# Optimization experiments

Hardware: AMD Instinct MI355X
Metric: run time of the kernel (lower is better)

Reference implementation:

```python
import jax, jax.numpy as jnp
import numpy as np

D_MODEL = 768
NUM_HEADS = 12
HEAD_DIM = D_MODEL // NUM_HEADS
LN_EPS = 1e-5
MASK_NEG = -1000000.0


def setup_inputs() -> dict:
    key = jax.random.key(0)
    ks = jax.random.split(key, 10)
    B, L, S = 2, 2048, 2048
    s = 1.0 / np.sqrt(D_MODEL)
    return {
        "q": jax.random.normal(ks[0], (B, L, D_MODEL), jnp.float32),
        "k": jax.random.normal(ks[1], (B, S, D_MODEL), jnp.float32),
        "v": jax.random.normal(ks[2], (B, S, D_MODEL), jnp.float32),
        "attention_mask": jnp.ones((B, S), jnp.int32),
        "Wq": jax.random.normal(ks[3], (D_MODEL, D_MODEL), jnp.float32) * s,
        "Wk": jax.random.normal(ks[4], (D_MODEL, D_MODEL), jnp.float32) * s,
        "Wv": jax.random.normal(ks[5], (D_MODEL, D_MODEL), jnp.float32) * s,
        "W": jax.random.normal(ks[6], (D_MODEL, D_MODEL), jnp.float32) * s,
        "b": jnp.zeros((D_MODEL,), jnp.float32),
        "gamma": jnp.ones((D_MODEL,), jnp.float32),
        "beta": jnp.zeros((D_MODEL,), jnp.float32),
    }


def reference(q, k, v, attention_mask, Wq, Wk, Wv, W, b, gamma, beta):
    B, L, D = q.shape
    S = k.shape[1]
    H, hd = NUM_HEADS, HEAD_DIM
    # projections (torch Linear: x @ W^T), split heads -> (B,H,L,hd)
    Q = (q @ Wq.T).reshape(B, L, H, hd).transpose(0, 2, 1, 3)
    K = (k @ Wk.T).reshape(B, S, H, hd).transpose(0, 2, 1, 3)
    V = (v @ Wv.T).reshape(B, S, H, hd).transpose(0, 2, 1, 3)
    # scores (B,H,L,S) with additive key-padding mask
    scores = jnp.einsum("bhld,bhsd->bhls", Q, K) / np.sqrt(hd)
    mask_score = (1.0 - attention_mask.astype(q.dtype))[:, None, None, :] * MASK_NEG
    att = jax.nn.softmax(scores + mask_score, axis=-1)  # dropout p=0 (eval)
    # attend, merge heads, output projection (with bias)
    O = jnp.einsum("bhls,bhsd->bhld", att, V).transpose(0, 2, 1, 3).reshape(B, L, D)
    O = O @ W.T + b  # state dropout p=0 (eval)
    # residual + LayerNorm
    x = q + O
    mu = jnp.mean(x, axis=-1, keepdims=True)
    var = jnp.mean(jnp.square(x - mu), axis=-1, keepdims=True)
    return (x - mu) * jax.lax.rsqrt(var + LN_EPS) * gamma + beta
```

## Files before the change

kernel.cpp:

```cpp
#include <hip/hip_runtime.h>
#include <hip/hip_bf16.h>
#include <math.h>


typedef unsigned short u16;
typedef unsigned int   u32;
typedef __bf16 bf16x8 __attribute__((ext_vector_type(8)));
typedef float  f32x4  __attribute__((ext_vector_type(4)));

#define DM   768
#define MR   4096
#define WSZ  589824

#define LOG2E 1.44269504089f
#define SM_C  15.0f
#define K1    (0.125f * LOG2E)

__device__ inline u16 bfbits(float f) {
    union { __bf16 b; u16 u; } x; x.b = (__bf16)f; return x.u;
}

__device__ inline uint4 cvt8(const float* src) {
    const float4* p = reinterpret_cast<const float4*>(src);
    float4 a = p[0], b = p[1];
    union { __bf16 h[8]; uint4 v; } u;
    u.h[0] = (__bf16)a.x; u.h[1] = (__bf16)a.y; u.h[2] = (__bf16)a.z; u.h[3] = (__bf16)a.w;
    u.h[4] = (__bf16)b.x; u.h[5] = (__bf16)b.y; u.h[6] = (__bf16)b.z; u.h[7] = (__bf16)b.w;
    return u.v;
}

__global__ __launch_bounds__(256) void wcvt(
    const float* __restrict__ w0, const float* __restrict__ w1,
    const float* __restrict__ w2, const float* __restrict__ w3,
    u16* __restrict__ dst)
{
    const float* src = (blockIdx.y == 0) ? w0 : (blockIdx.y == 1) ? w1
                     : (blockIdx.y == 2) ? w2 : w3;
    size_t idx = ((size_t)blockIdx.x * 256 + threadIdx.x) * 8;
    *reinterpret_cast<uint4*>(&dst[(size_t)blockIdx.y * WSZ + idx]) = cvt8(&src[idx]);
}

__global__ __launch_bounds__(256) void gemm_qkv(
    const float* __restrict__ xq, const float* __restrict__ xk, const float* __restrict__ xv,
    const u16* __restrict__ Wb4,
    u16* __restrict__ oq, u16* __restrict__ ok, u16* __restrict__ ov)
{
    const int mode = blockIdx.z;
    const float* X = (mode == 0) ? xq : (mode == 1) ? xk : xv;
    const u16* Wb  = Wb4 + (size_t)mode * WSZ;
    u16* out       = (mode == 0) ? oq : (mode == 1) ? ok : ov;

    __shared__ __attribute__((aligned(16))) u16 As[64][72];
    __shared__ __attribute__((aligned(16))) u16 Bs[64][72];

    const int tid  = threadIdx.x;
    const int lane = tid & 63;
    const int w    = tid >> 6;
    const int wm   = (w >> 1) * 32;
    const int wn   = (w & 1) * 32;
    const int quad = lane >> 4;
    const int l16  = lane & 15;
    const int tm   = blockIdx.x * 64;
    const int tn   = blockIdx.y * 64;

    f32x4 acc[2][2] = {};

    for (int k0 = 0; k0 < 768; k0 += 64) {
        __syncthreads();
        #pragma unroll
        for (int rep = 0; rep < 2; rep++) {
            int idx = tid + rep * 256;
            int row = idx >> 3;
            int col = (idx & 7) * 8;
            *reinterpret_cast<uint4*>(&As[row][col]) = cvt8(&X[(size_t)(tm + row) * 768 + k0 + col]);
            *reinterpret_cast<uint4*>(&Bs[row][col]) =
                *reinterpret_cast<const uint4*>(&Wb[(size_t)(tn + row) * 768 + k0 + col]);
        }
        __syncthreads();
        #pragma unroll
        for (int kk = 0; kk < 2; kk++) {
            bf16x8 a0 = *reinterpret_cast<const bf16x8*>(&As[wm + l16     ][kk*32 + quad*8]);
            bf16x8 a1 = *reinterpret_cast<const bf16x8*>(&As[wm + 16 + l16][kk*32 + quad*8]);
            bf16x8 b0 = *reinterpret_cast<const bf16x8*>(&Bs[wn + l16     ][kk*32 + quad*8]);
            bf16x8 b1 = *reinterpret_cast<const bf16x8*>(&Bs[wn + 16 + l16][kk*32 + quad*8]);
            acc[0][0] = __builtin_amdgcn_mfma_f32_16x16x32_bf16(a0, b0, acc[0][0], 0, 0, 0);
            acc[0][1] = __builtin_amdgcn_mfma_f32_16x16x32_bf16(a0, b1, acc[0][1], 0, 0, 0);
            acc[1][0] = __builtin_amdgcn_mfma_f32_16x16x32_bf16(a1, b0, acc[1][0], 0, 0, 0);
            acc[1][1] = __builtin_amdgcn_mfma_f32_16x16x32_bf16(a1, b1, acc[1][1], 0, 0, 0);
        }
    }

    #pragma unroll
    for (int i = 0; i < 2; i++)
        #pragma unroll
        for (int j = 0; j < 2; j++)
            #pragma unroll
            for (int r = 0; r < 4; r++) {
                int gm = tm + wm + i * 16 + quad * 4 + r;
                int gn = tn + wn + j * 16 + l16;
                int b = gm >> 11, l = gm & 2047;
                int h = gn >> 6,  d = gn & 63;
                u16 bv = bfbits(acc[i][j][r]);
                if (mode == 2)
                    out[((size_t)(b * 12 + h) * 64 + d) * 2048 + l] = bv;
                else
                    out[((size_t)(b * 12 + h) * 2048 + l) * 64 + d] = bv;
            }
}

__global__ __launch_bounds__(256) void gemm_out(
    const u16* __restrict__ Oa, const u16* __restrict__ Wb,
    const float* __restrict__ bias, const float* __restrict__ resid,
    float* __restrict__ Xb)
{
    __shared__ __attribute__((aligned(16))) u16 As[64][72];
    __shared__ __attribute__((aligned(16))) u16 Bs[64][72];

    const int tid  = threadIdx.x;
    const int lane = tid & 63;
    const int w    = tid >> 6;
    const int wm   = (w >> 1) * 32;
    const int wn   = (w & 1) * 32;
    const int quad = lane >> 4;
    const int l16  = lane & 15;
    const int tm   = blockIdx.x * 64;
    const int tn   = blockIdx.y * 64;

    f32x4 acc[2][2] = {};

    for (int k0 = 0; k0 < 768; k0 += 64) {
        __syncthreads();
        #pragma unroll
        for (int rep = 0; rep < 2; rep++) {
            int idx = tid + rep * 256;
            int row = idx >> 3;
            int col = (idx & 7) * 8;
            *reinterpret_cast<uint4*>(&As[row][col]) =
                *reinterpret_cast<const uint4*>(&Oa[(size_t)(tm + row) * 768 + k0 + col]);
            *reinterpret_cast<uint4*>(&Bs[row][col]) =
                *reinterpret_cast<const uint4*>(&Wb[(size_t)(tn + row) * 768 + k0 + col]);
        }
        __syncthreads();
        #pragma unroll
        for (int kk = 0; kk < 2; kk++) {
            bf16x8 a0 = *reinterpret_cast<const bf16x8*>(&As[wm + l16     ][kk*32 + quad*8]);
            bf16x8 a1 = *reinterpret_cast<const bf16x8*>(&As[wm + 16 + l16][kk*32 + quad*8]);
            bf16x8 b0 = *reinterpret_cast<const bf16x8*>(&Bs[wn + l16     ][kk*32 + quad*8]);
            bf16x8 b1 = *reinterpret_cast<const bf16x8*>(&Bs[wn + 16 + l16][kk*32 + quad*8]);
            acc[0][0] = __builtin_amdgcn_mfma_f32_16x16x32_bf16(a0, b0, acc[0][0], 0, 0, 0);
            acc[0][1] = __builtin_amdgcn_mfma_f32_16x16x32_bf16(a0, b1, acc[0][1], 0, 0, 0);
            acc[1][0] = __builtin_amdgcn_mfma_f32_16x16x32_bf16(a1, b0, acc[1][0], 0, 0, 0);
            acc[1][1] = __builtin_amdgcn_mfma_f32_16x16x32_bf16(a1, b1, acc[1][1], 0, 0, 0);
        }
    }

    #pragma unroll
    for (int i = 0; i < 2; i++)
        #pragma unroll
        for (int j = 0; j < 2; j++)
            #pragma unroll
            for (int r = 0; r < 4; r++) {
                int gm = tm + wm + i * 16 + quad * 4 + r;
                int gn = tn + wn + j * 16 + l16;
                Xb[(size_t)gm * 768 + gn] = acc[i][j][r] + bias[gn] + resid[(size_t)gm * 768 + gn];
            }
}

__global__ __launch_bounds__(256) void attn(
    const u16* __restrict__ Qp, const u16* __restrict__ Kp, const u16* __restrict__ Vt,
    const int* __restrict__ amask, u16* __restrict__ Oatt)
{
    __shared__ __attribute__((aligned(16))) u16 Ks[128][72];
    __shared__ __attribute__((aligned(16))) u16 Vs[64][136];
    __shared__ __attribute__((aligned(16))) u16 Ps[4][16][72];
    __shared__ float maskC[2048];

    const int tid  = threadIdx.x;
    const int lane = tid & 63;
    const int w    = tid >> 6;
    const int quad = lane >> 4;
    const int l16  = lane & 15;
    const int qt = blockIdx.x;
    const int h  = blockIdx.y;
    const int b  = blockIdx.z;

    #pragma unroll
    for (int i = 0; i < 8; i++) {
        int s = tid + i * 256;
        maskC[s] = amask[b * 2048 + s] ? (-SM_C * LOG2E) : -2.0e6f;
    }

    const u16* Qbase = Qp + ((size_t)(b * 12 + h) * 2048 + qt * 64) * 64;
    const u16* Kbase = Kp + (size_t)(b * 12 + h) * 2048 * 64;
    const u16* Vbase = Vt + (size_t)(b * 12 + h) * 64 * 2048;

    bf16x8 qfrag[2];
    #pragma unroll
    for (int kk = 0; kk < 2; kk++)
        qfrag[kk] = *reinterpret_cast<const bf16x8*>(&Qbase[(w * 16 + l16) * 64 + kk * 32 + quad * 8]);

    bf16x8 onesf = {};
    if (l16 == 0) {
        #pragma unroll
        for (int i = 0; i < 8; i++) onesf[i] = (__bf16)1.0f;
    }

    const int krow = tid >> 1,  kcb = (tid & 1) * 32;
    const int vrow = tid >> 2,  vcb = (tid & 3) * 32;

    f32x4 oacc[4] = {};
    f32x4 sacc = {};

    for (int st = 0; st < 16; st++) {
        __syncthreads();
        #pragma unroll
        for (int i = 0; i < 4; i++)
            *reinterpret_cast<uint4*>(&Ks[krow][kcb + i * 8]) =
                *reinterpret_cast<const uint4*>(
                    &Kbase[(size_t)(st * 128 + krow) * 64 + kcb + i * 8]);
        #pragma unroll
        for (int i = 0; i < 4; i++)
            *reinterpret_cast<uint4*>(&Vs[vrow][vcb + i * 8]) =
                *reinterpret_cast<const uint4*>(
                    &Vbase[(size_t)vrow * 2048 + st * 128 + vcb + i * 8]);
        __syncthreads();

        #pragma unroll
        for (int h2 = 0; h2 < 2; h2++) {
            const int kb = h2 * 64;
            #pragma unroll
            for (int ct = 0; ct < 4; ct++) {
                f32x4 s = {};
                #pragma unroll
                for (int kk = 0; kk < 2; kk++) {
                    bf16x8 kf = *reinterpret_cast<const bf16x8*>(
                        &Ks[kb + ct * 16 + l16][kk * 32 + quad * 8]);
                    s = __builtin_amdgcn_mfma_f32_16x16x32_bf16(qfrag[kk], kf, s, 0, 0, 0);
                }
                float cc = maskC[st * 128 + kb + ct * 16 + l16];
                #pragma unroll
                for (int r = 0; r < 4; r++) {
                    float p = __builtin_amdgcn_exp2f(__builtin_fmaf(s[r], K1, cc));
                    Ps[w][quad * 4 + r][ct * 16 + l16] = bfbits(p);
                }
            }
            bf16x8 pf[2];
            #pragma unroll
            for (int kk = 0; kk < 2; kk++)
                pf[kk] = *reinterpret_cast<const bf16x8*>(&Ps[w][l16][kk * 32 + quad * 8]);
            #pragma unroll
            for (int kk = 0; kk < 2; kk++)
                sacc = __builtin_amdgcn_mfma_f32_16x16x32_bf16(pf[kk], onesf, sacc, 0, 0, 0);
            #pragma unroll
            for (int ct = 0; ct < 4; ct++)
                #pragma unroll
                for (int kk = 0; kk < 2; kk++) {
                    bf16x8 vf = *reinterpret_cast<const bf16x8*>(
                        &Vs[ct * 16 + l16][kb + kk * 32 + quad * 8]);
                    oacc[ct] = __builtin_amdgcn_mfma_f32_16x16x32_bf16(pf[kk], vf, oacc[ct], 0, 0, 0);
                }
        }
    }

    float rinv[4];
    #pragma unroll
    for (int r = 0; r < 4; r++) {
        float ls = __shfl(sacc[r], lane & 48, 64);
        rinv[r] = 1.0f / ls;
    }
    #pragma unroll
    for (int ct = 0; ct < 4; ct++)
        #pragma unroll
        for (int r = 0; r < 4; r++) {
            int grow = b * 2048 + qt * 64 + w * 16 + quad * 4 + r;
            int gcol = h * 64 + ct * 16 + l16;
            Oatt[(size_t)grow * 768 + gcol] = bfbits(oacc[ct][r] * rinv[r]);
        }
}

__global__ __launch_bounds__(256) void ln_kernel(
    float* __restrict__ X, const float* __restrict__ gamma,
    const float* __restrict__ beta)
{
    const int row = blockIdx.x;
    const int tid = threadIdx.x;
    float* xr = X + (size_t)row * 768;

    float v[3], s = 0.f, s2 = 0.f;
    #pragma unroll
    for (int i = 0; i < 3; i++) {
        v[i] = xr[tid + i * 256];
        s += v[i];
        s2 += v[i] * v[i];
    }
    #pragma unroll
    for (int off = 32; off >= 1; off >>= 1) {
        s  += __shfl_xor(s,  off, 64);
        s2 += __shfl_xor(s2, off, 64);
    }
    __shared__ float rs[4], rs2[4];
    int w = tid >> 6, lane = tid & 63;
    if (lane == 0) { rs[w] = s; rs2[w] = s2; }
    __syncthreads();
    s  = rs[0] + rs[1] + rs[2] + rs[3];
    s2 = rs2[0] + rs2[1] + rs2[2] + rs2[3];
    float mu = s * (1.0f / 768.0f);
    float var = s2 * (1.0f / 768.0f) - mu * mu;
    float rstd = rsqrtf(var + 1e-5f);
    #pragma unroll
    for (int i = 0; i < 3; i++) {
        int c = tid + i * 256;
        xr[c] = (v[i] - mu) * rstd * gamma[c] + beta[c];
    }
}

extern "C" void kernel_launch(void* const* d_in, const int* in_sizes, int n_in,
                              void* d_out, int out_size, void* d_ws, size_t ws_size,
                              hipStream_t stream)
{
    const float* q   = (const float*)d_in[0];
    const float* k   = (const float*)d_in[1];
    const float* v   = (const float*)d_in[2];
    const int*   am  = (const int*)d_in[3];
    const float* Wq  = (const float*)d_in[4];
    const float* Wk  = (const float*)d_in[5];
    const float* Wv  = (const float*)d_in[6];
    const float* W   = (const float*)d_in[7];
    const float* bb  = (const float*)d_in[8];
    const float* gam = (const float*)d_in[9];
    const float* bet = (const float*)d_in[10];

    u16* Wb4 = (u16*)d_ws;
    u16* Qp  = Wb4 + (size_t)4 * WSZ;
    u16* Kp  = Qp + (size_t)MR * DM;
    u16* Vt  = Kp + (size_t)MR * DM;
    u16* Oa  = Vt + (size_t)MR * DM;
    float* Xb = (float*)d_out;

    wcvt<<<dim3(288, 4), 256, 0, stream>>>(Wq, Wk, Wv, W, Wb4);
    gemm_qkv<<<dim3(64, 12, 3), 256, 0, stream>>>(q, k, v, Wb4, Qp, Kp, Vt);
    attn<<<dim3(32, 12, 2), 256, 0, stream>>>(Qp, Kp, Vt, am, Oa);
    gemm_out<<<dim3(64, 12), 256, 0, stream>>>(Oa, Wb4 + (size_t)3 * WSZ, bb, q, Xb);
    ln_kernel<<<4096, 256, 0, stream>>>(Xb, gam, bet);
}
```

Before: 246.5 us.

## Split attention keys across waves with direct register loads and LDS reduction

The attention kernel now gives each wave all 64 query rows and its own 32-key slice of every 128-key tile. Each wave loads its K and V fragments straight from global memory into registers, so the shared K/V staging and the two barriers per tile are gone. The per-wave partial outputs and row sums are then added together in shared memory over four serialized passes before normalizing and writing out. This removes LDS staging traffic and in-loop synchronization, but adds a serialized cross-wave reduction, uses many more accumulator registers (occupancy hint set to 3), and relies on uncoalesced global fragment loads.

```diff
diff --git a/kernel.cpp b/kernel.cpp
--- a/kernel.cpp
+++ b/kernel.cpp
@@ -166,14 +166,14 @@
             }
 }
 
-__global__ __launch_bounds__(256) void attn(
+__global__ __launch_bounds__(256, 3) void attn(
     const u16* __restrict__ Qp, const u16* __restrict__ Kp, const u16* __restrict__ Vt,
     const int* __restrict__ amask, u16* __restrict__ Oatt)
 {
-    __shared__ __attribute__((aligned(16))) u16 Ks[128][72];
-    __shared__ __attribute__((aligned(16))) u16 Vs[64][136];
-    __shared__ __attribute__((aligned(16))) u16 Ps[4][16][72];
-    __shared__ float maskC[2048];
+    __shared__ __attribute__((aligned(16))) unsigned char smem[4 * 64 * 40 * 2 + 2048 * 4];
+    u16 (*Ps)[64][40] = reinterpret_cast<u16(*)[64][40]>(smem);
+    float* maskC = reinterpret_cast<float*>(smem + 20480);
+    float (*Obuf)[72] = reinterpret_cast<float(*)[72]>(smem);
 
     const int tid  = threadIdx.x;
     const int lane = tid & 63;
@@ -189,15 +189,19 @@
         int s = tid + i * 256;
         maskC[s] = amask[b * 2048 + s] ? (-SM_C * LOG2E) : -2.0e6f;
     }
+    __syncthreads();
 
     const u16* Qbase = Qp + ((size_t)(b * 12 + h) * 2048 + qt * 64) * 64;
-    const u16* Kbase = Kp + (size_t)(b * 12 + h) * 2048 * 64;
-    const u16* Vbase = Vt + (size_t)(b * 12 + h) * 64 * 2048;
-
-    bf16x8 qfrag[2];
-    #pragma unroll
-    for (int kk = 0; kk < 2; kk++)
-        qfrag[kk] = *reinterpret_cast<const bf16x8*>(&Qbase[(w * 16 + l16) * 64 + kk * 32 + quad * 8]);
+    const u16* Kb2   = Kp + (size_t)(b * 12 + h) * 2048 * 64 + (size_t)w * 32 * 64;
+    const u16* Vb2   = Vt + (size_t)(b * 12 + h) * 64 * 2048 + (size_t)w * 32;
+
+    bf16x8 qfrag[4][2];
+    #pragma unroll
+    for (int qb = 0; qb < 4; qb++)
+        #pragma unroll
+        for (int kk = 0; kk < 2; kk++)
+            qfrag[qb][kk] = *reinterpret_cast<const bf16x8*>(
+                &Qbase[(qb * 16 + l16) * 64 + kk * 32 + quad * 8]);
 
     bf16x8 onesf = {};
     if (l16 == 0) {
@@ -205,77 +209,93 @@
         for (int i = 0; i < 8; i++) onesf[i] = (__bf16)1.0f;
     }
 
-    const int krow = tid >> 1,  kcb = (tid & 1) * 32;
-    const int vrow = tid >> 2,  vcb = (tid & 3) * 32;
-
-    f32x4 oacc[4] = {};
-    f32x4 sacc = {};
+    f32x4 oacc[4][4] = {};
+    f32x4 sacc[4]    = {};
 
     for (int st = 0; st < 16; st++) {
-        __syncthreads();
-        #pragma unroll
-        for (int i = 0; i < 4; i++)
-            *reinterpret_cast<uint4*>(&Ks[krow][kcb + i * 8]) =
-                *reinterpret_cast<const uint4*>(
-                    &Kbase[(size_t)(st * 128 + krow) * 64 + kcb + i * 8]);
-        #pragma unroll
-        for (int i = 0; i < 4; i++)
-            *reinterpret_cast<uint4*>(&Vs[vrow][vcb + i * 8]) =
-                *reinterpret_cast<const uint4*>(
-                    &Vbase[(size_t)vrow * 2048 + st * 128 + vcb + i * 8]);
-        __syncthreads();
-
-        #pragma unroll
-        for (int h2 = 0; h2 < 2; h2++) {
-            const int kb = h2 * 64;
-            #pragma unroll
-            for (int ct = 0; ct < 4; ct++) {
+        bf16x8 kf[2][2], vf[4];
+        #pragma unroll
+        for (int ct = 0; ct < 2; ct++)
+            #pragma unroll
+            for (int kk = 0; kk < 2; kk++)
+                kf[ct][kk] = *reinterpret_cast<const bf16x8*>(
+                    &Kb2[(size_t)(st * 128 + ct * 16 + l16) * 64 + kk * 32 + quad * 8]);
+        #pragma unroll
+        for (int cd = 0; cd < 4; cd++)
+            vf[cd] = *reinterpret_cast<const bf16x8*>(
+                &Vb2[(size_t)(cd * 16 + l16) * 2048 + st * 128 + quad * 8]);
+
+        float cc0 = maskC[st * 128 + w * 32 + l16];
+        float cc1 = maskC[st * 128 + w * 32 + 16 + l16];
+
+        #pragma unroll
+        for (int qb = 0; qb < 4; qb++)
+            #pragma unroll
+            for (int ct = 0; ct < 2; ct++) {
                 f32x4 s = {};
-                #pragma unroll
-                for (int kk = 0; kk < 2; kk++) {
-                    bf16x8 kf = *reinterpret_cast<const bf16x8*>(
-                        &Ks[kb + ct * 16 + l16][kk * 32 + quad * 8]);
-                    s = __builtin_amdgcn_mfma_f32_16x16x32_bf16(qfrag[kk], kf, s, 0, 0, 0);
-                }
-                float cc = maskC[st * 128 + kb + ct * 16 + l16];
+                s = __builtin_amdgcn_mfma_f32_16x16x32_bf16(qfrag[qb][0], kf[ct][0], s, 0, 0, 0);
+                s = __builtin_amdgcn_mfma_f32_16x16x32_bf16(qfrag[qb][1], kf[ct][1], s, 0, 0, 0);
+                float cc = ct ? cc1 : cc0;
                 #pragma unroll
                 for (int r = 0; r < 4; r++) {
                     float p = __builtin_amdgcn_exp2f(__builtin_fmaf(s[r], K1, cc));
-                    Ps[w][quad * 4 + r][ct * 16 + l16] = bfbits(p);
+                    Ps[w][qb * 16 + quad * 4 + r][ct * 16 + l16] = bfbits(p);
                 }
             }
-            bf16x8 pf[2];
-            #pragma unroll
-            for (int kk = 0; kk < 2; kk++)
-                pf[kk] = *reinterpret_cast<const bf16x8*>(&Ps[w][l16][kk * 32 + quad * 8]);
-            #pragma unroll
-            for (int kk = 0; kk < 2; kk++)
-                sacc = __builtin_amdgcn_mfma_f32_16x16x32_bf16(pf[kk], onesf, sacc, 0, 0, 0);
-            #pragma unroll
-            for (int ct = 0; ct < 4; ct++)
+
+        bf16x8 pf[4];
+        #pragma unroll
+        for (int qb = 0; qb < 4; qb++)
+            pf[qb] = *reinterpret_cast<const bf16x8*>(&Ps[w][qb * 16 + l16][quad * 8]);
+        #pragma unroll
+        for (int qb = 0; qb < 4; qb++)
+            sacc[qb] = __builtin_amdgcn_mfma_f32_16x16x32_bf16(pf[qb], onesf, sacc[qb], 0, 0, 0);
+        #pragma unroll
+        for (int qb = 0; qb < 4; qb++)
+            #pragma unroll
+            for (int cd = 0; cd < 4; cd++)
+                oacc[qb][cd] = __builtin_amdgcn_mfma_f32_16x16x32_bf16(pf[qb], vf[cd], oacc[qb][cd], 0, 0, 0);
+    }
+
+    __syncthreads();
+    for (int wv = 0; wv < 4; wv++) {
+        if (w == wv) {
+            #pragma unroll
+            for (int qb = 0; qb < 4; qb++) {
                 #pragma unroll
-                for (int kk = 0; kk < 2; kk++) {
-                    bf16x8 vf = *reinterpret_cast<const bf16x8*>(
-                        &Vs[ct * 16 + l16][kb + kk * 32 + quad * 8]);
-                    oacc[ct] = __builtin_amdgcn_mfma_f32_16x16x32_bf16(pf[kk], vf, oacc[ct], 0, 0, 0);
+                for (int cd = 0; cd < 4; cd++)
+                    #pragma unroll
+                    for (int r = 0; r < 4; r++) {
+                        float* cell = &Obuf[qb * 16 + quad * 4 + r][cd * 16 + l16];
+                        if (wv == 0) *cell = oacc[qb][cd][r];
+                        else         *cell += oacc[qb][cd][r];
+                    }
+                if (l16 == 0) {
+                    #pragma unroll
+                    for (int r = 0; r < 4; r++) {
+                        float* cell = &Obuf[qb * 16 + quad * 4 + r][64];
+                        if (wv == 0) *cell = sacc[qb][r];
+                        else         *cell += sacc[qb][r];
+                    }
                 }
-        }
-    }
-
-    float rinv[4];
-    #pragma unroll
-    for (int r = 0; r < 4; r++) {
-        float ls = __shfl(sacc[r], lane & 48, 64);
-        rinv[r] = 1.0f / ls;
-    }
-    #pragma unroll
-    for (int ct = 0; ct < 4; ct++)
-        #pragma unroll
-        for (int r = 0; r < 4; r++) {
-            int grow = b * 2048 + qt * 64 + w * 16 + quad * 4 + r;
-            int gcol = h * 64 + ct * 16 + l16;
-            Oatt[(size_t)grow * 768 + gcol] = bfbits(oacc[ct][r] * rinv[r]);
-        }
+            }
+        }
+        __syncthreads();
+    }
+
+    #pragma unroll
+    for (int g = 0; g < 4; g++) {
+        int unit = tid + g * 256;
+        int row = unit >> 4;
+        int c4  = (unit & 15) * 4;
+        float rinv = 1.0f / Obuf[row][64];
+        union { u16 h[4]; uint2 v; } o;
+        #pragma unroll
+        for (int j = 0; j < 4; j++)
+            o.h[j] = bfbits(Obuf[row][c4 + j] * rinv);
+        *reinterpret_cast<uint2*>(
+            &Oatt[(size_t)(b * 2048 + qt * 64 + row) * 768 + h * 64 + c4]) = o.v;
+    }
 }
 
 __global__ __launch_bounds__(256) void ln_kernel(
```

Result: faster. 226.3 us (-8.2%).
